# Optimization experiments

Hardware: AMD Instinct MI355X
Metric: run time of the kernel (lower is better)

Reference implementation:

```python
import jax, jax.numpy as jnp
import numpy as np

E = 500_000
B = 64
N_INC = 64
E_INC = 64
U_INC = 64
W_INC = 2
H1 = 128   # edge_model_mlp1_hidden_sizes[0]
H2 = 128   # edge_model_mlp1_hidden_sizes[1] == GRU hidden
E_OUT = 64
DIM_IN = E_INC + 2 * N_INC + U_INC      # 256
DIM_W2 = DIM_IN // 2                     # 128
DIM_X1 = DIM_IN + DIM_W2                 # 384
LN_EPS = 1e-5


def _layernorm(x, g, b):
    mu = jnp.mean(x, axis=-1, keepdims=True)
    var = jnp.mean(jnp.square(x - mu), axis=-1, keepdims=True)
    return (x - mu) * jax.lax.rsqrt(var + LN_EPS) * g + b


def setup_inputs() -> dict:
    key = jax.random.key(0)
    ks = jax.random.split(key, 20)
    s = lambda k, shape: (jax.random.normal(k, shape, dtype=jnp.float32) * 0.05)
    return {
        "src": jax.random.normal(ks[0], (E, N_INC), dtype=jnp.float32),
        "dest": jax.random.normal(ks[1], (E, N_INC), dtype=jnp.float32),
        "edge_attr": jax.random.normal(ks[2], (E, E_INC), dtype=jnp.float32),
        "h": jax.random.normal(ks[3], (E, H2), dtype=jnp.float32),
        "u": jax.random.normal(ks[4], (B, U_INC), dtype=jnp.float32),
        "batch": jax.random.randint(ks[5], (E,), 0, B, dtype=jnp.int32),
        "winding": jax.random.uniform(ks[6], (E, W_INC), dtype=jnp.float32),
        # winding_mlp: Linear(W_INC, DIM_W2) + LayerNorm
        "Ww": s(ks[7], (DIM_W2, W_INC)),
        "bw": jnp.zeros((DIM_W2,), jnp.float32),
        "gw": jnp.ones((DIM_W2,), jnp.float32),
        "betaw": jnp.zeros((DIM_W2,), jnp.float32),
        # mlp1: Linear(DIM_X1, H1) + LayerNorm
        "W1": s(ks[8], (H1, DIM_X1)),
        "b1": jnp.zeros((H1,), jnp.float32),
        "g1": jnp.ones((H1,), jnp.float32),
        "beta1": jnp.zeros((H1,), jnp.float32),
        # GRU(H1 -> H2), 1 layer
        "Wih": s(ks[9], (3 * H2, H1)),
        "Whh": s(ks[10], (3 * H2, H2)),
        "bih": jnp.zeros((3 * H2,), jnp.float32),
        "bhh": jnp.zeros((3 * H2,), jnp.float32),
        # mlp_x: Linear(H2, E_OUT)
        "Wx": s(ks[11], (E_OUT, H2)),
        "bx": jnp.zeros((E_OUT,), jnp.float32),
    }


def reference(src, dest, edge_attr, h, u, batch, winding,
              Ww, bw, gw, betaw, W1, b1, g1, beta1,
              Wih, Whh, bih, bhh, Wx, bx):
    # winding_mlp: Linear + LayerNorm + ReLU
    w = jax.nn.relu(_layernorm(winding @ Ww.T + bw, gw, betaw))      # [E, DIM_W2]
    # concat [src, dest, edge_attr, u[batch], w]
    x = jnp.concatenate([src, dest, edge_attr, u[batch], w], axis=1)  # [E, DIM_X1]
    # mlp1: Linear + LayerNorm + ReLU
    x = jax.nn.relu(_layernorm(x @ W1.T + b1, g1, beta1))             # [E, H1]
    # single-step GRU (PyTorch gate order: r, z, n)
    gi = x @ Wih.T + bih                                              # [E, 3*H2]
    gh = h @ Whh.T + bhh                                              # [E, 3*H2]
    i_r, i_z, i_n = jnp.split(gi, 3, axis=-1)
    h_r, h_z, h_n = jnp.split(gh, 3, axis=-1)
    r = jax.nn.sigmoid(i_r + h_r)
    z = jax.nn.sigmoid(i_z + h_z)
    n = jnp.tanh(i_n + r * h_n)
    h_new = (1.0 - z) * n + z * h                                     # [E, H2]
    x_out = h_new @ Wx.T + bx                                         # [E, E_OUT]
    return (x_out, h_new)
```

## Files before the change

### kernel.cpp

```cpp
#include <hip/hip_runtime.h>
#include <hip/hip_bf16.h>

#define E_TOTAL 500000
#define NB2 7813
#define NTIL 7813
#define GBLK 256

typedef __attribute__((ext_vector_type(8))) short bf16x8;
typedef __attribute__((ext_vector_type(4))) float f32x4;

#define MFMA(a, b, c) __builtin_amdgcn_mfma_f32_16x16x32_bf16((a), (b), (c), 0, 0, 0)

typedef __attribute__((address_space(1))) const void GV;
typedef __attribute__((address_space(3))) void LV;

__device__ __forceinline__ void lbar() {
    asm volatile("s_waitcnt lgkmcnt(0)" ::: "memory");
    __builtin_amdgcn_s_barrier();
}
__device__ __forceinline__ unsigned int pack2(float x, float y) {
    unsigned int xb = __builtin_bit_cast(unsigned int, x) + 0x8000u;
    unsigned int yb = __builtin_bit_cast(unsigned int, y) + 0x8000u;
    return __builtin_amdgcn_perm(yb, xb, 0x07060302u);
}
__device__ __forceinline__ float sigm(float x) { return 1.f / (1.f + __expf(-x)); }
__device__ __forceinline__ float tanh_fast(float x) {
    float t = __expf(-2.f * x);
    return (1.f - t) / (1.f + t);
}
__device__ __forceinline__ char* swzp(void* base, int row, int rowBytes, int colByte) {
    return (char*)base + row * rowBytes + (colByte ^ ((row & 7) << 4));
}

__global__ void wconv_kernel(const float* __restrict__ W1, const float* __restrict__ Wih,
                             const float* __restrict__ Whh, const float* __restrict__ Wx,
                             unsigned short* __restrict__ out) {
    int i = blockIdx.x * 256 + threadIdx.x;
    if (i >= 155648) return;
    float v;
    if      (i < 49152)  v = W1[i];
    else if (i < 98304)  v = Wih[i - 49152];
    else if (i < 147456) v = Whh[i - 98304];
    else                 v = Wx[i - 147456];
    unsigned int b = __builtin_bit_cast(unsigned int, v) + 0x8000u;
    out[i] = (unsigned short)(b >> 16);
}

struct SmemM {
    unsigned short x1[64][384];
    float lns[64][4];
    float ln2[64][4];
    float par[640];
};

__global__ __launch_bounds__(256) void mlp1_kernel(
    const float* __restrict__ src, const float* __restrict__ dst,
    const float* __restrict__ eat, const float* __restrict__ u,
    const int* __restrict__ batch, const float* __restrict__ winding,
    const float* __restrict__ Ww, const float* __restrict__ bw,
    const float* __restrict__ gw, const float* __restrict__ betaw,
    const float* __restrict__ b1, const float* __restrict__ g1,
    const float* __restrict__ beta1,
    const unsigned short* __restrict__ W1bf,
    unsigned short* __restrict__ ybf)
{
    __shared__ SmemM sm;
    const int tid  = threadIdx.x;
    const int wave = tid >> 6;
    const int lane = tid & 63;
    const int lhi  = lane >> 4;
    const int llo  = lane & 15;
    const size_t e0 = (size_t)blockIdx.x * 64;

    for (int i = tid; i < 640; i += 256) {
        float v;
        if      (i < 256) v = Ww[i];
        else if (i < 384) v = bw[i - 256];
        else if (i < 512) v = gw[i - 384];
        else              v = betaw[i - 512];
        sm.par[i] = v;
    }
    lbar();

    #pragma unroll
    for (int it = 0; it < 4; ++it) {
        int q   = it * 256 + tid;
        int row = q >> 4;
        int c4  = (q & 15) << 2;
        size_t e = e0 + row; if (e >= E_TOTAL) e = E_TOTAL - 1;
        float4 a = *(const float4*)(src + e * 64 + c4);
        float4 b = *(const float4*)(dst + e * 64 + c4);
        float4 c = *(const float4*)(eat + e * 64 + c4);
        int bi   = batch[e];
        float4 d = *(const float4*)(u + (size_t)bi * 64 + c4);
        uint2 pa = make_uint2(pack2(a.x, a.y), pack2(a.z, a.w));
        uint2 pb = make_uint2(pack2(b.x, b.y), pack2(b.z, b.w));
        uint2 pc = make_uint2(pack2(c.x, c.y), pack2(c.z, c.w));
        uint2 pd = make_uint2(pack2(d.x, d.y), pack2(d.z, d.w));
        *(uint2*)swzp(sm.x1, row, 768, 2 * c4)       = pa;
        *(uint2*)swzp(sm.x1, row, 768, 128 + 2 * c4) = pb;
        *(uint2*)swzp(sm.x1, row, 768, 256 + 2 * c4) = pc;
        *(uint2*)swzp(sm.x1, row, 768, 384 + 2 * c4) = pd;
    }
    {
        int row = tid >> 2;
        int seg = tid & 3;
        size_t e = e0 + row; if (e >= E_TOTAL) e = E_TOTAL - 1;
        float wi0 = winding[e * 2], wi1 = winding[e * 2 + 1];
        float vals[32]; float s = 0.f, s2 = 0.f;
        #pragma unroll
        for (int j = 0; j < 32; ++j) {
            int jj = seg * 32 + j;
            float v = fmaf(wi0, sm.par[2 * jj], fmaf(wi1, sm.par[2 * jj + 1], sm.par[256 + jj]));
            vals[j] = v; s += v; s2 += v * v;
        }
        s  += __shfl_xor(s, 1);  s  += __shfl_xor(s, 2);
        s2 += __shfl_xor(s2, 1); s2 += __shfl_xor(s2, 2);
        float mean = s * (1.f / 128.f);
        float var  = fmaxf(s2 * (1.f / 128.f) - mean * mean, 0.f);
        float inv  = rsqrtf(var + 1e-5f);
        #pragma unroll
        for (int j4 = 0; j4 < 8; ++j4) {
            int jj = seg * 32 + j4 * 4;
            float v0 = fmaxf((vals[j4*4+0] - mean) * inv * sm.par[384 + jj]     + sm.par[512 + jj],     0.f);
            float v1 = fmaxf((vals[j4*4+1] - mean) * inv * sm.par[384 + jj + 1] + sm.par[512 + jj + 1], 0.f);
            float v2 = fmaxf((vals[j4*4+2] - mean) * inv * sm.par[384 + jj + 2] + sm.par[512 + jj + 2], 0.f);
            float v3 = fmaxf((vals[j4*4+3] - mean) * inv * sm.par[384 + jj + 3] + sm.par[512 + jj + 3], 0.f);
            uint2 pk = make_uint2(pack2(v0, v1), pack2(v2, v3));
            *(uint2*)swzp(sm.x1, row, 768, 512 + seg * 64 + j4 * 8) = pk;
        }
    }
    lbar();

    f32x4 acc[2][4];
    #pragma unroll
    for (int nt = 0; nt < 2; ++nt)
        #pragma unroll
        for (int mt = 0; mt < 4; ++mt) acc[nt][mt] = (f32x4){0.f, 0.f, 0.f, 0.f};
    {
        const unsigned short* wp = W1bf + (size_t)(wave * 32 + llo) * 384 + lhi * 8;
        #pragma unroll
        for (int ks = 0; ks < 12; ++ks) {
            bf16x8 wf0 = *(const bf16x8*)(wp + ks * 32);
            bf16x8 wf1 = *(const bf16x8*)(wp + 16 * 384 + ks * 32);
            #pragma unroll
            for (int mt = 0; mt < 4; ++mt) {
                bf16x8 xf = *(const bf16x8*)swzp(sm.x1, mt * 16 + llo, 768, ks * 64 + lhi * 16);
                acc[0][mt] = MFMA(wf0, xf, acc[0][mt]);
                acc[1][mt] = MFMA(wf1, xf, acc[1][mt]);
            }
        }
    }
    {
        float4 b1q0 = *(const float4*)&b1[wave * 32 + lhi * 4];
        float4 b1q1 = *(const float4*)&b1[wave * 32 + 16 + lhi * 4];
        #pragma unroll
        for (int mt = 0; mt < 4; ++mt) {
            float s = 0.f, s2 = 0.f;
            #pragma unroll
            for (int r = 0; r < 4; ++r) {
                float v0 = acc[0][mt][r] + ((const float*)&b1q0)[r];
                float v1 = acc[1][mt][r] + ((const float*)&b1q1)[r];
                acc[0][mt][r] = v0; acc[1][mt][r] = v1;
                s += v0 + v1; s2 += v0 * v0 + v1 * v1;
            }
            s  += __shfl_xor(s, 16);  s  += __shfl_xor(s, 32);
            s2 += __shfl_xor(s2, 16); s2 += __shfl_xor(s2, 32);
            if (lane < 16) { sm.lns[mt * 16 + llo][wave] = s; sm.ln2[mt * 16 + llo][wave] = s2; }
        }
    }
    lbar();

    {
        float4 g1q0  = *(const float4*)&g1[wave * 32 + lhi * 4];
        float4 g1q1  = *(const float4*)&g1[wave * 32 + 16 + lhi * 4];
        float4 be1q0 = *(const float4*)&beta1[wave * 32 + lhi * 4];
        float4 be1q1 = *(const float4*)&beta1[wave * 32 + 16 + lhi * 4];
        #pragma unroll
        for (int mt = 0; mt < 4; ++mt) {
            int edge = mt * 16 + llo;
            size_t e = e0 + edge;
            float4 sa = *(const float4*)&sm.lns[edge][0];
            float4 ta = *(const float4*)&sm.ln2[edge][0];
            float s  = sa.x + sa.y + sa.z + sa.w;
            float s2 = ta.x + ta.y + ta.z + ta.w;
            float mean = s * (1.f / 128.f);
            float var  = fmaxf(s2 * (1.f / 128.f) - mean * mean, 0.f);
            float inv  = rsqrtf(var + 1e-5f);
            if (e < E_TOTAL) {
                #pragma unroll
                for (int nt = 0; nt < 2; ++nt) {
                    const float4& gq  = nt ? g1q1 : g1q0;
                    const float4& beq = nt ? be1q1 : be1q0;
                    float v0 = fmaxf((acc[nt][mt][0] - mean) * inv * gq.x + beq.x, 0.f);
                    float v1 = fmaxf((acc[nt][mt][1] - mean) * inv * gq.y + beq.y, 0.f);
                    float v2 = fmaxf((acc[nt][mt][2] - mean) * inv * gq.z + beq.z, 0.f);
                    float v3 = fmaxf((acc[nt][mt][3] - mean) * inv * gq.w + beq.w, 0.f);
                    uint2 pk = make_uint2(pack2(v0, v1), pack2(v2, v3));
                    int f = wave * 32 + nt * 16 + lhi * 4;
                    *(uint2*)(ybf + e * 128 + f) = pk;
                }
            }
        }
    }
}

__global__ __launch_bounds__(512, 1) void gru_kernel(
    const unsigned short* __restrict__ ybf, const float* __restrict__ hin,
    const float* __restrict__ bih, const float* __restrict__ bhh,
    const float* __restrict__ bx,
    const unsigned short* __restrict__ Wihbf, const unsigned short* __restrict__ Whhbf,
    const unsigned short* __restrict__ Wxbf,
    float* __restrict__ xout, float* __restrict__ hout)
{
    __shared__ unsigned short smy[2][64][128];
    __shared__ float          smh[2][64][128];
    const int tid  = threadIdx.x;
    const int wave = tid >> 6;
    const int lane = tid & 63;
    const int lhi  = lane >> 4;
    const int llo  = lane & 15;
    const int f    = wave * 16 + lhi * 4;
    const int fx   = (wave & 3) * 16 + lhi * 4;
    const int eh   = (wave >> 2) * 32;

    const float4 bi0 = *(const float4*)&bih[f];
    const float4 bi1 = *(const float4*)&bih[128 + f];
    const float4 bi2 = *(const float4*)&bih[256 + f];
    const float4 bh0 = *(const float4*)&bhh[f];
    const float4 bh1 = *(const float4*)&bhh[128 + f];
    const float4 bh2 = *(const float4*)&bhh[256 + f];
    const float4 bxq = *(const float4*)&bx[fx];
    const unsigned short* pi = Wihbf + (size_t)(wave * 16 + llo) * 128 + lhi * 8;
    const unsigned short* pw = Whhbf + (size_t)(wave * 16 + llo) * 128 + lhi * 8;
    const unsigned short* px = Wxbf + (size_t)((wave & 3) * 16 + llo) * 128 + lhi * 8;

    auto stage = [&](int t, int buf) {
        const size_t eb = (size_t)t * 64;
        #pragma unroll
        for (int j = 0; j < 2; ++j) {
            int O = j * 8192 + tid * 16;
            int row = O >> 8, colB = O & 255;
            size_t e = eb + row; if (e >= E_TOTAL) e = E_TOTAL - 1;
            unsigned lc = (unsigned)colB ^ (((unsigned)row & 7u) << 4);
            const char* gp = (const char*)ybf + e * 256 + lc;
            char* lp = (char*)&smy[buf][0][0] + O;
            __builtin_amdgcn_global_load_lds((GV*)gp, (LV*)lp, 16, 0, 0);
        }
        #pragma unroll
        for (int j = 0; j < 4; ++j) {
            int O = j * 8192 + tid * 16;
            int row = O >> 9, colB = O & 511;
            size_t e = eb + row; if (e >= E_TOTAL) e = E_TOTAL - 1;
            unsigned lc = (unsigned)colB ^ (((unsigned)row & 7u) << 4);
            const char* gp = (const char*)hin + e * 512 + lc;
            char* lp = (char*)&smh[buf][0][0] + O;
            __builtin_amdgcn_global_load_lds((GV*)gp, (LV*)lp, 16, 0, 0);
        }
    };

    int cur = 0;
    stage(blockIdx.x, 0);
    asm volatile("s_waitcnt vmcnt(0)" ::: "memory");
    lbar();

    for (int t = blockIdx.x; t < NTIL; t += GBLK) {
        const size_t e0 = (size_t)t * 64;
        {
            int tn = t + GBLK; if (tn >= NTIL) tn = t;
            stage(tn, cur ^ 1);
        }

        f32x4 gr[4], gz[4], gn[4], gh[4];
        #pragma unroll
        for (int mt = 0; mt < 4; ++mt) {
            gr[mt] = (f32x4){0.f,0.f,0.f,0.f}; gz[mt] = (f32x4){0.f,0.f,0.f,0.f};
            gn[mt] = (f32x4){0.f,0.f,0.f,0.f}; gh[mt] = (f32x4){0.f,0.f,0.f,0.f};
        }
        #pragma unroll
        for (int ks = 0; ks < 4; ++ks) {
            bf16x8 wr = *(const bf16x8*)(pi + ks * 32);
            bf16x8 wz = *(const bf16x8*)(pi + 128 * 128 + ks * 32);
            bf16x8 wn = *(const bf16x8*)(pi + 256 * 128 + ks * 32);
            bf16x8 vr = *(const bf16x8*)(pw + ks * 32);
            bf16x8 vz = *(const bf16x8*)(pw + 128 * 128 + ks * 32);
            bf16x8 vn = *(const bf16x8*)(pw + 256 * 128 + ks * 32);
            #pragma unroll
            for (int mt = 0; mt < 4; ++mt) {
                int row = mt * 16 + llo;
                bf16x8 ay = *(const bf16x8*)swzp(smy[cur], row, 256, ks * 64 + lhi * 16);
                float4 q0 = *(const float4*)swzp(smh[cur], row, 512, ks * 128 + lhi * 32);
                float4 q1 = *(const float4*)swzp(smh[cur], row, 512, ks * 128 + lhi * 32 + 16);
                uint4 up;
                up.x = pack2(q0.x, q0.y); up.y = pack2(q0.z, q0.w);
                up.z = pack2(q1.x, q1.y); up.w = pack2(q1.z, q1.w);
                bf16x8 ah = __builtin_bit_cast(bf16x8, up);
                gr[mt] = MFMA(wr, ay, gr[mt]);  gr[mt] = MFMA(vr, ah, gr[mt]);
                gz[mt] = MFMA(wz, ay, gz[mt]);  gz[mt] = MFMA(vz, ah, gz[mt]);
                gn[mt] = MFMA(wn, ay, gn[mt]);  gh[mt] = MFMA(vn, ah, gh[mt]);
            }
        }
        lbar();

        #pragma unroll
        for (int mt = 0; mt < 4; ++mt) {
            int row = mt * 16 + llo;
            float4 hv = *(const float4*)swzp(smh[cur], row, 512, 4 * f);
            float4 ho;
            #pragma unroll
            for (int r = 0; r < 4; ++r) {
                float rr = sigm(gr[mt][r] + ((const float*)&bi0)[r] + ((const float*)&bh0)[r]);
                float zz = sigm(gz[mt][r] + ((const float*)&bi1)[r] + ((const float*)&bh1)[r]);
                float nn = tanh_fast(gn[mt][r] + ((const float*)&bi2)[r]
                                     + rr * (gh[mt][r] + ((const float*)&bh2)[r]));
                ((float*)&ho)[r] = (1.f - zz) * nn + zz * ((const float*)&hv)[r];
            }
            ushort4 pk;
            pk.x = (unsigned short)(pack2(ho.x, ho.y) & 0xffffu);
            pk.y = (unsigned short)(pack2(ho.x, ho.y) >> 16);
            pk.z = (unsigned short)(pack2(ho.z, ho.w) & 0xffffu);
            pk.w = (unsigned short)(pack2(ho.z, ho.w) >> 16);
            *(ushort4*)swzp(smy[cur], row, 256, 2 * f) = pk;
            size_t e = e0 + row;
            if (e < E_TOTAL) *(float4*)(hout + e * 128 + f) = ho;
        }
        lbar();

        {
            f32x4 a3[2];
            a3[0] = (f32x4){0.f,0.f,0.f,0.f}; a3[1] = (f32x4){0.f,0.f,0.f,0.f};
            #pragma unroll
            for (int ks = 0; ks < 4; ++ks) {
                bf16x8 wf = *(const bf16x8*)(px + ks * 32);
                #pragma unroll
                for (int mt = 0; mt < 2; ++mt) {
                    bf16x8 bh = *(const bf16x8*)swzp(smy[cur], eh + mt * 16 + llo, 256, ks * 64 + lhi * 16);
                    a3[mt] = MFMA(wf, bh, a3[mt]);
                }
            }
            #pragma unroll
            for (int mt = 0; mt < 2; ++mt) {
                size_t e = e0 + eh + mt * 16 + llo;
                float4 o;
                o.x = a3[mt][0] + bxq.x; o.y = a3[mt][1] + bxq.y;
                o.z = a3[mt][2] + bxq.z; o.w = a3[mt][3] + bxq.w;
                if (e < E_TOTAL) *(float4*)(xout + e * 64 + fx) = o;
            }
        }

        asm volatile("s_waitcnt vmcnt(6)" ::: "memory");
        lbar();
        cur ^= 1;
    }
}

extern "C" void kernel_launch(void* const* d_in, const int* in_sizes, int n_in,
                              void* d_out, int out_size, void* d_ws, size_t ws_size,
                              hipStream_t stream)
{
    const float* src   = (const float*)d_in[0];
    const float* dst   = (const float*)d_in[1];
    const float* eat   = (const float*)d_in[2];
    const float* hin   = (const float*)d_in[3];
    const float* u     = (const float*)d_in[4];
    const int*   bat   = (const int*)d_in[5];
    const float* wind  = (const float*)d_in[6];
    const float* Ww    = (const float*)d_in[7];
    const float* bw    = (const float*)d_in[8];
    const float* gw    = (const float*)d_in[9];
    const float* betaw = (const float*)d_in[10];
    const float* W1    = (const float*)d_in[11];
    const float* b1    = (const float*)d_in[12];
    const float* g1    = (const float*)d_in[13];
    const float* beta1 = (const float*)d_in[14];
    const float* Wih   = (const float*)d_in[15];
    const float* Whh   = (const float*)d_in[16];
    const float* bih   = (const float*)d_in[17];
    const float* bhh   = (const float*)d_in[18];
    const float* Wx    = (const float*)d_in[19];
    const float* bx    = (const float*)d_in[20];

    unsigned short* ybf  = (unsigned short*)d_ws;
    unsigned short* wbuf = ybf + 64000000ull;

    wconv_kernel<<<608, 256, 0, stream>>>(W1, Wih, Whh, Wx, wbuf);

    float* xout = (float*)d_out;
    float* hout = xout + (size_t)E_TOTAL * 64;

    mlp1_kernel<<<NB2, 256, 0, stream>>>(
        src, dst, eat, u, bat, wind, Ww, bw, gw, betaw,
        b1, g1, beta1, wbuf, ybf);

    gru_kernel<<<GBLK, 512, 0, stream>>>(
        ybf, hin, bih, bhh, bx,
        wbuf + 49152, wbuf + 98304, wbuf + 147456,
        xout, hout);
}
```

Before: 582.5 us.

## Pre-convert hidden state to bf16 in mlp1 and double GRU occupancy

The mlp1 kernel now also reads the fp32 hidden state and writes a bf16 copy into the xout region of the output buffer, which the GRU kernel later overwrites tile by tile. The GRU kernel stages bf16 h through LDS, which halves its h staging size and removes in-loop packing. It also writes the new h into a separate LDS buffer so one barrier can go, folds the r/z biases together, and doubles the grid with two blocks per CU. The costs are an extra pass over h in mlp1, reduced precision of h in the z*h blend, and reliance on the aliased scratch being consumed before the same tile's xout is written.

```diff
diff --git a/kernel.cpp b/kernel.cpp
--- a/kernel.cpp
+++ b/kernel.cpp
@@ -4,7 +4,7 @@
 #define E_TOTAL 500000
 #define NB2 7813
 #define NTIL 7813
-#define GBLK 256
+#define GBLK 512
 
 typedef __attribute__((ext_vector_type(8))) short bf16x8;
 typedef __attribute__((ext_vector_type(4))) float f32x4;
@@ -22,6 +22,9 @@
     unsigned int xb = __builtin_bit_cast(unsigned int, x) + 0x8000u;
     unsigned int yb = __builtin_bit_cast(unsigned int, y) + 0x8000u;
     return __builtin_amdgcn_perm(yb, xb, 0x07060302u);
+}
+__device__ __forceinline__ float b2f(unsigned short s) {
+    return __bfloat162float(__builtin_bit_cast(__hip_bfloat16, s));
 }
 __device__ __forceinline__ float sigm(float x) { return 1.f / (1.f + __expf(-x)); }
 __device__ __forceinline__ float tanh_fast(float x) {
@@ -57,12 +60,13 @@
     const float* __restrict__ src, const float* __restrict__ dst,
     const float* __restrict__ eat, const float* __restrict__ u,
     const int* __restrict__ batch, const float* __restrict__ winding,
+    const float* __restrict__ hin,
     const float* __restrict__ Ww, const float* __restrict__ bw,
     const float* __restrict__ gw, const float* __restrict__ betaw,
     const float* __restrict__ b1, const float* __restrict__ g1,
     const float* __restrict__ beta1,
     const unsigned short* __restrict__ W1bf,
-    unsigned short* __restrict__ ybf)
+    unsigned short* __restrict__ ybf, unsigned short* __restrict__ hbf)
 {
     __shared__ SmemM sm;
     const int tid  = threadIdx.x;
@@ -101,6 +105,20 @@
         *(uint2*)swzp(sm.x1, row, 768, 128 + 2 * c4) = pb;
         *(uint2*)swzp(sm.x1, row, 768, 256 + 2 * c4) = pc;
         *(uint2*)swzp(sm.x1, row, 768, 384 + 2 * c4) = pd;
+    }
+    #pragma unroll
+    for (int it = 0; it < 4; ++it) {
+        int q   = it * 256 + tid;
+        int row = q >> 4;
+        int c8  = (q & 15) << 3;
+        size_t e = e0 + row;
+        size_t ec = e < E_TOTAL ? e : E_TOTAL - 1;
+        float4 a = *(const float4*)(hin + ec * 128 + c8);
+        float4 b = *(const float4*)(hin + ec * 128 + c8 + 4);
+        uint4 pk;
+        pk.x = pack2(a.x, a.y); pk.y = pack2(a.z, a.w);
+        pk.z = pack2(b.x, b.y); pk.w = pack2(b.z, b.w);
+        if (e < E_TOTAL) *(uint4*)(hbf + e * 128 + c8) = pk;
     }
     {
         int row = tid >> 2;
@@ -205,16 +223,17 @@
     }
 }
 
-__global__ __launch_bounds__(512, 1) void gru_kernel(
-    const unsigned short* __restrict__ ybf, const float* __restrict__ hin,
+__global__ __launch_bounds__(512, 2) void gru_kernel(
+    const unsigned short* __restrict__ ybf, const unsigned short* hbf,
     const float* __restrict__ bih, const float* __restrict__ bhh,
     const float* __restrict__ bx,
     const unsigned short* __restrict__ Wihbf, const unsigned short* __restrict__ Whhbf,
     const unsigned short* __restrict__ Wxbf,
-    float* __restrict__ xout, float* __restrict__ hout)
+    float* xout, float* __restrict__ hout)
 {
     __shared__ unsigned short smy[2][64][128];
-    __shared__ float          smh[2][64][128];
+    __shared__ unsigned short smh[2][64][128];
+    __shared__ unsigned short smn[64][128];
     const int tid  = threadIdx.x;
     const int wave = tid >> 6;
     const int lane = tid & 63;
@@ -224,11 +243,14 @@
     const int fx   = (wave & 3) * 16 + lhi * 4;
     const int eh   = (wave >> 2) * 32;
 
-    const float4 bi0 = *(const float4*)&bih[f];
-    const float4 bi1 = *(const float4*)&bih[128 + f];
+    float4 br_, bz_;
+    {
+        float4 a0 = *(const float4*)&bih[f],       c0 = *(const float4*)&bhh[f];
+        float4 a1 = *(const float4*)&bih[128 + f], c1 = *(const float4*)&bhh[128 + f];
+        br_.x = a0.x + c0.x; br_.y = a0.y + c0.y; br_.z = a0.z + c0.z; br_.w = a0.w + c0.w;
+        bz_.x = a1.x + c1.x; bz_.y = a1.y + c1.y; bz_.z = a1.z + c1.z; bz_.w = a1.w + c1.w;
+    }
     const float4 bi2 = *(const float4*)&bih[256 + f];
-    const float4 bh0 = *(const float4*)&bhh[f];
-    const float4 bh1 = *(const float4*)&bhh[128 + f];
     const float4 bh2 = *(const float4*)&bhh[256 + f];
     const float4 bxq = *(const float4*)&bx[fx];
     const unsigned short* pi = Wihbf + (size_t)(wave * 16 + llo) * 128 + lhi * 8;
@@ -243,19 +265,10 @@
             int row = O >> 8, colB = O & 255;
             size_t e = eb + row; if (e >= E_TOTAL) e = E_TOTAL - 1;
             unsigned lc = (unsigned)colB ^ (((unsigned)row & 7u) << 4);
-            const char* gp = (const char*)ybf + e * 256 + lc;
-            char* lp = (char*)&smy[buf][0][0] + O;
-            __builtin_amdgcn_global_load_lds((GV*)gp, (LV*)lp, 16, 0, 0);
-        }
-        #pragma unroll
-        for (int j = 0; j < 4; ++j) {
-            int O = j * 8192 + tid * 16;
-            int row = O >> 9, colB = O & 511;
-            size_t e = eb + row; if (e >= E_TOTAL) e = E_TOTAL - 1;
-            unsigned lc = (unsigned)colB ^ (((unsigned)row & 7u) << 4);
-            const char* gp = (const char*)hin + e * 512 + lc;
-            char* lp = (char*)&smh[buf][0][0] + O;
-            __builtin_amdgcn_global_load_lds((GV*)gp, (LV*)lp, 16, 0, 0);
+            __builtin_amdgcn_global_load_lds((GV*)((const char*)ybf + e * 256 + lc),
+                                             (LV*)((char*)&smy[buf][0][0] + O), 16, 0, 0);
+            __builtin_amdgcn_global_load_lds((GV*)((const char*)hbf + e * 256 + lc),
+                                             (LV*)((char*)&smh[buf][0][0] + O), 16, 0, 0);
         }
     };
 
@@ -289,38 +302,32 @@
             for (int mt = 0; mt < 4; ++mt) {
                 int row = mt * 16 + llo;
                 bf16x8 ay = *(const bf16x8*)swzp(smy[cur], row, 256, ks * 64 + lhi * 16);
-                float4 q0 = *(const float4*)swzp(smh[cur], row, 512, ks * 128 + lhi * 32);
-                float4 q1 = *(const float4*)swzp(smh[cur], row, 512, ks * 128 + lhi * 32 + 16);
-                uint4 up;
-                up.x = pack2(q0.x, q0.y); up.y = pack2(q0.z, q0.w);
-                up.z = pack2(q1.x, q1.y); up.w = pack2(q1.z, q1.w);
-                bf16x8 ah = __builtin_bit_cast(bf16x8, up);
+                bf16x8 ah = *(const bf16x8*)swzp(smh[cur], row, 256, ks * 64 + lhi * 16);
                 gr[mt] = MFMA(wr, ay, gr[mt]);  gr[mt] = MFMA(vr, ah, gr[mt]);
                 gz[mt] = MFMA(wz, ay, gz[mt]);  gz[mt] = MFMA(vz, ah, gz[mt]);
                 gn[mt] = MFMA(wn, ay, gn[mt]);  gh[mt] = MFMA(vn, ah, gh[mt]);
             }
         }
-        lbar();
 
         #pragma unroll
         for (int mt = 0; mt < 4; ++mt) {
             int row = mt * 16 + llo;
-            float4 hv = *(const float4*)swzp(smh[cur], row, 512, 4 * f);
+            ushort4 hp = *(const ushort4*)swzp(smh[cur], row, 256, 2 * f);
             float4 ho;
             #pragma unroll
             for (int r = 0; r < 4; ++r) {
-                float rr = sigm(gr[mt][r] + ((const float*)&bi0)[r] + ((const float*)&bh0)[r]);
-                float zz = sigm(gz[mt][r] + ((const float*)&bi1)[r] + ((const float*)&bh1)[r]);
+                float rr = sigm(gr[mt][r] + ((const float*)&br_)[r]);
+                float zz = sigm(gz[mt][r] + ((const float*)&bz_)[r]);
                 float nn = tanh_fast(gn[mt][r] + ((const float*)&bi2)[r]
                                      + rr * (gh[mt][r] + ((const float*)&bh2)[r]));
-                ((float*)&ho)[r] = (1.f - zz) * nn + zz * ((const float*)&hv)[r];
-            }
+                float hv = b2f(((const unsigned short*)&hp)[r]);
+                ((float*)&ho)[r] = (1.f - zz) * nn + zz * hv;
+            }
+            unsigned int p0 = pack2(ho.x, ho.y), p1 = pack2(ho.z, ho.w);
             ushort4 pk;
-            pk.x = (unsigned short)(pack2(ho.x, ho.y) & 0xffffu);
-            pk.y = (unsigned short)(pack2(ho.x, ho.y) >> 16);
-            pk.z = (unsigned short)(pack2(ho.z, ho.w) & 0xffffu);
-            pk.w = (unsigned short)(pack2(ho.z, ho.w) >> 16);
-            *(ushort4*)swzp(smy[cur], row, 256, 2 * f) = pk;
+            pk.x = (unsigned short)(p0 & 0xffffu); pk.y = (unsigned short)(p0 >> 16);
+            pk.z = (unsigned short)(p1 & 0xffffu); pk.w = (unsigned short)(p1 >> 16);
+            *(ushort4*)swzp(smn, row, 256, 2 * f) = pk;
             size_t e = e0 + row;
             if (e < E_TOTAL) *(float4*)(hout + e * 128 + f) = ho;
         }
@@ -334,7 +341,7 @@
                 bf16x8 wf = *(const bf16x8*)(px + ks * 32);
                 #pragma unroll
                 for (int mt = 0; mt < 2; ++mt) {
-                    bf16x8 bh = *(const bf16x8*)swzp(smy[cur], eh + mt * 16 + llo, 256, ks * 64 + lhi * 16);
+                    bf16x8 bh = *(const bf16x8*)swzp(smn, eh + mt * 16 + llo, 256, ks * 64 + lhi * 16);
                     a3[mt] = MFMA(wf, bh, a3[mt]);
                 }
             }
@@ -348,7 +355,8 @@
             }
         }
 
-        asm volatile("s_waitcnt vmcnt(6)" ::: "memory");
+        if (e0 + 64 <= E_TOTAL) asm volatile("s_waitcnt vmcnt(6)" ::: "memory");
+        else                    asm volatile("s_waitcnt vmcnt(0)" ::: "memory");
         lbar();
         cur ^= 1;
     }
@@ -383,17 +391,18 @@
     unsigned short* ybf  = (unsigned short*)d_ws;
     unsigned short* wbuf = ybf + 64000000ull;
 
-    wconv_kernel<<<608, 256, 0, stream>>>(W1, Wih, Whh, Wx, wbuf);
-
     float* xout = (float*)d_out;
     float* hout = xout + (size_t)E_TOTAL * 64;
+    unsigned short* hbf = (unsigned short*)d_out;
+
+    wconv_kernel<<<608, 256, 0, stream>>>(W1, Wih, Whh, Wx, wbuf);
 
     mlp1_kernel<<<NB2, 256, 0, stream>>>(
-        src, dst, eat, u, bat, wind, Ww, bw, gw, betaw,
-        b1, g1, beta1, wbuf, ybf);
+        src, dst, eat, u, bat, wind, hin, Ww, bw, gw, betaw,
+        b1, g1, beta1, wbuf, ybf, hbf);
 
     gru_kernel<<<GBLK, 512, 0, stream>>>(
-        ybf, hin, bih, bhh, bx,
+        ybf, hbf, bih, bhh, bx,
         wbuf + 49152, wbuf + 98304, wbuf + 147456,
         xout, hout);
 }
```

After: 503.7 us. -13.5%, faster.
